# Kernel tuning notes

Measured on AMD Instinct MI355X. Metric: run time of the kernel, lower is better.

Reference implementation:

```python
import jax, jax.numpy as jnp
import numpy as np

LATENT, U_DIM, NUM_PROD, NUM_INJ, FEAT_C = 128, 30, 20, 10, 128
WELL_IN = LATENT + U_DIM + FEAT_C  # 286
HID = 64
B = 16384


def setup_inputs() -> dict:
    key = jax.random.key(0)
    ks = jax.random.split(key, 12)
    s = lambda fan_in: 1.0 / np.sqrt(fan_in)
    return {
        "zt": jax.random.normal(ks[0], (B, LATENT), jnp.float32),
        "dt": 1,
        "ut": jax.random.normal(ks[1], (B, U_DIM), jnp.float32),
        "well_features": jax.random.normal(ks[2], (B, NUM_PROD, FEAT_C), jnp.float32),
        # StructuredODEFunc params: dz/dt = -(L L^T) z + Bm u
        "L": jax.random.normal(ks[3], (LATENT, LATENT), jnp.float32) * s(LATENT),
        "Bm": jax.random.normal(ks[4], (LATENT, U_DIM), jnp.float32) * s(U_DIM),
        # per-well MLP heads, stacked: [P, in, out]
        "W1": jax.random.uniform(ks[5], (NUM_PROD, WELL_IN, HID), jnp.float32, -s(WELL_IN), s(WELL_IN)),
        "b1": jax.random.uniform(ks[6], (NUM_PROD, HID), jnp.float32, -s(WELL_IN), s(WELL_IN)),
        "W2": jax.random.uniform(ks[7], (NUM_PROD, HID, 2), jnp.float32, -s(HID), s(HID)),
        "b2": jax.random.uniform(ks[8], (NUM_PROD, 2), jnp.float32, -s(HID), s(HID)),
        # injector head: Linear(latent+u_dim, num_inj)
        "Wi": jax.random.uniform(ks[9], (LATENT + U_DIM, NUM_INJ), jnp.float32, -s(LATENT + U_DIM), s(LATENT + U_DIM)),
        "bi": jax.random.uniform(ks[10], (NUM_INJ,), jnp.float32, -s(LATENT + U_DIM), s(LATENT + U_DIM)),
    }


def reference(zt, dt, ut, well_features, L, Bm, W1, b1, W2, b2, Wi, bi):
    # ODE step: A = -L L^T, f(z) = A z + Bm u; euler over t_span [0,1] -> one step h=1
    A = -(L @ L.T)                                  # [D, D]
    zt1 = zt + zt @ A.T + ut @ Bm.T                 # [B, D]
    zu = jnp.concatenate([zt1, ut], axis=-1)        # [B, D+U]
    # per-well heads, fused as batched gather-MLP
    zu_b = jnp.broadcast_to(zu[:, None, :], (zu.shape[0], NUM_PROD, zu.shape[1]))
    head_in = jnp.concatenate([zu_b, well_features], axis=-1)        # [B, P, WELL_IN]
    h = jax.nn.relu(jnp.einsum('bpi,pih->bph', head_in, W1) + b1)    # [B, P, 64]
    well_out = jnp.einsum('bph,pho->bpo', h, W2) + b2                # [B, P, 2]
    well_out = well_out.reshape(well_out.shape[0], NUM_PROD * 2)     # concat order matches loop
    inj_out = zu @ Wi + bi                                           # [B, num_inj]
    yt1 = jnp.concatenate([well_out, inj_out], axis=-1)              # [B, 2P+I]
    return zt1, yt1
```

## Files before the change

kernel.cpp:

```cpp
#include <hip/hip_runtime.h>

#define BATCH   16384
#define LATENT  128
#define U_DIM   30
#define NUM_PROD 20
#define NUM_INJ 10
#define FEAT_C  128
#define WELL_IN 286
#define HID     64
#define ZT1_N   (BATCH*LATENT)
#define OUT_ROW (NUM_PROD*2+NUM_INJ)

typedef unsigned short u16;
typedef __attribute__((ext_vector_type(8))) short  short8;
typedef __attribute__((ext_vector_type(4))) float  floatx4;

__device__ __forceinline__ u16 f2bf(float f){
    unsigned x = __builtin_bit_cast(unsigned, f);
    x += 0x7fffu + ((x >> 16) & 1u);
    return (u16)(x >> 16);
}
__device__ __forceinline__ short8 cvt8(floatx4 a, floatx4 b){
    short8 s;
    s[0]=(short)f2bf(a[0]); s[1]=(short)f2bf(a[1]);
    s[2]=(short)f2bf(a[2]); s[3]=(short)f2bf(a[3]);
    s[4]=(short)f2bf(b[0]); s[5]=(short)f2bf(b[1]);
    s[6]=(short)f2bf(b[2]); s[7]=(short)f2bf(b[3]);
    return s;
}

#define NW1  368640
#define NGS  20480
#define NWIS 2560
#define NW2S 20480
__device__ u16 g_w1s[NW1];
__device__ u16 g_gs [NGS];
__device__ u16 g_wis[NWIS];
__device__ u16 g_w2s[NW2S];

__global__ __launch_bounds__(256) void prep_kernel(
    const float* __restrict__ L, const float* __restrict__ Bm,
    const float* __restrict__ W1, const float* __restrict__ Wi,
    const float* __restrict__ W2)
{
    const int bx = blockIdx.x, t = threadIdx.x;
    if (bx < 180) {
        int s = bx*256 + t;
        int lane = s & 63;
        int rest = s >> 6;
        int kk = rest % 9, pn = rest / 9;
        int n0 = pn & 3, p = pn >> 2;
        int kbase = kk*32 + ((lane>>4)*8);
        int n = n0*16 + (lane & 15);
        short8 v;
#pragma unroll
        for (int j = 0; j < 8; j++) {
            int k = kbase + j;
            u16 b = 0;
            if (k < 158)        b = f2bf(W1[(p*WELL_IN + k)*HID + n]);
            else if (k >= 160)  b = f2bf(W1[(p*WELL_IN + (k-2))*HID + n]);
            v[j] = (short)b;
        }
        *(short8*)&g_w1s[(size_t)s*8] = v;
        return;
    }
    if (bx < 272) {
        int sid = (bx-180)*256 + t;
        if (sid < NW2S) {
            int j=sid&7, lane=(sid>>3)&63, rest=sid>>9;
            int kk=rest&1, p=rest>>1;
            int k=kk*32+((lane>>4)*8)+j, n=lane&15;
            g_w2s[sid] = (n<2) ? f2bf(W2[(p*HID+k)*2+n]) : (u16)0;
            return;
        }
        sid -= NW2S;
        if (sid < NWIS) {
            int j=sid&7, lane=(sid>>3)&63, kk=sid>>9;
            int k=kk*32+((lane>>4)*8)+j, n=lane&15;
            g_wis[sid] = (k<158 && n<NUM_INJ) ? f2bf(Wi[k*NUM_INJ+n]) : (u16)0;
            return;
        }
        sid -= NWIS;
        if (sid < 512) {
            int lane=sid&63, nt=sid>>6;
            int q=lane>>4, n=nt*16+(lane&15);
#pragma unroll
            for (int j = 0; j < 8; j++) {
                int u = q*8 + j;
                float v = (u < U_DIM) ? Bm[n*U_DIM + u] : 0.f;
                g_gs[((nt*5+4)*64 + lane)*8 + j] = f2bf(v);
            }
        }
        return;
    }
    const int mt = bx - 272;
    const int w = t>>6, lane=t&63, q=lane>>4, m=lane&15;
    floatx4 accG[2];
    accG[0]=(floatx4){0.f,0.f,0.f,0.f}; accG[1]=(floatx4){0.f,0.f,0.f,0.f};
#pragma unroll
    for (int kk = 0; kk < 4; kk++) {
        const float* ap = &L[(mt*16+m)*128 + kk*32 + q*8];
        short8 a = cvt8(*(const floatx4*)ap, *(const floatx4*)(ap+4));
#pragma unroll
        for (int ntl = 0; ntl < 2; ntl++) {
            int nt = w*2 + ntl;
            const float* bp = &L[(nt*16+m)*128 + kk*32 + q*8];
            short8 b = cvt8(*(const floatx4*)bp, *(const floatx4*)(bp+4));
            accG[ntl] = __builtin_amdgcn_mfma_f32_16x16x32_bf16(a, b, accG[ntl], 0, 0, 0);
        }
    }
#pragma unroll
    for (int ntl = 0; ntl < 2; ntl++)
#pragma unroll
        for (int r = 0; r < 4; r++) {
            int kg = mt*16 + q*4 + r;
            int n  = (w*2+ntl)*16 + m;
            float v = ((kg==n) ? 1.f : 0.f) - accG[ntl][r];
            int fi = ((n>>4)*5 + (kg>>5))*512 + (((kg>>3)&3)*16 + (n&15))*8 + (kg&7);
            g_gs[fi] = f2bf(v);
        }
}

__global__ __launch_bounds__(256) void ker_main(
    const float* __restrict__ zt, const float* __restrict__ ut,
    const float* __restrict__ wff, const float* __restrict__ b1,
    const float* __restrict__ b2,  const float* __restrict__ bi,
    float* __restrict__ outf)
{
    __shared__ alignas(16) u16   zus[32][168];
    __shared__ alignas(16) u16   wfb0[4096];
    __shared__ alignas(16) u16   wfb1[4096];
    __shared__ alignas(16) u16   hs[32][72];
    __shared__ alignas(16) float outs[32][50];
    const int t = threadIdx.x;
    const int row0 = blockIdx.x * 32;
    const int w = t >> 6, lane = t & 63, q = lane >> 4, m = lane & 15;

    const int lane_s = t & 63, cs = (t >> 6) & 3;
    const int qs = lane_s >> 4, ms = lane_s & 15;

    floatx4 rA[4], rB[4];
    auto issue = [&](floatx4 (&r)[4], int p){
#pragma unroll
        for (int rt = 0; rt < 2; rt++) {
            const float* pb = &wff[((size_t)(row0 + rt*16 + ms)*NUM_PROD + p)*FEAT_C + cs*32 + qs*8];
            r[rt*2+0] = *(const floatx4*)pb;
            r[rt*2+1] = *(const floatx4*)(pb + 4);
        }
    };
    auto cstore = [&](const floatx4 (&r)[4], u16* __restrict__ wfb){
        *(short8*)&wfb[((size_t)(0*4 + cs)*64 + lane_s)*8] = cvt8(r[0], r[1]);
        *(short8*)&wfb[((size_t)(1*4 + cs)*64 + lane_s)*8] = cvt8(r[2], r[3]);
    };

    issue(rA, 0);
    issue(rB, 1);

    for (int i = t; i < 1024; i += 256) {
        int r = i >> 5, c4 = i & 31;
        floatx4 v = *(const floatx4*)&zt[(size_t)(row0 + r)*128 + c4*4];
        u16* d = &zus[r][c4*4];
        d[0]=f2bf(v[0]); d[1]=f2bf(v[1]); d[2]=f2bf(v[2]); d[3]=f2bf(v[3]);
    }
    for (int i = t; i < 32*U_DIM; i += 256) {
        int r = i / U_DIM, c = i - r*U_DIM;
        zus[r][128 + c] = f2bf(ut[(row0 + r)*U_DIM + c]);
    }
    if (t < 64) {
        zus[t >> 1][158 + (t & 1)] = 0;
    }
    __syncthreads();

    {
        const int mt = w & 1, ng = (w >> 1) * 4;
        floatx4 acc[4];
#pragma unroll
        for (int c = 0; c < 4; c++) acc[c] = (floatx4){0.f,0.f,0.f,0.f};
#pragma unroll
        for (int kk = 0; kk < 5; kk++) {
            short8 a = *(const short8*)&zus[mt*16 + m][kk*32 + q*8];
#pragma unroll
            for (int c = 0; c < 4; c++) {
                short8 b = *(const short8*)&g_gs[(((ng+c)*5 + kk)*64 + lane)*8];
                acc[c] = __builtin_amdgcn_mfma_f32_16x16x32_bf16(a, b, acc[c], 0, 0, 0);
            }
        }
        __syncthreads();
#pragma unroll
        for (int c = 0; c < 4; c++)
#pragma unroll
            for (int r = 0; r < 4; r++) {
                int row = mt*16 + q*4 + r;
                int col = (ng+c)*16 + m;
                float v = acc[c][r];
                outf[(size_t)(row0 + row)*128 + col] = v;
                zus[row][col] = f2bf(v);
            }
    }
    __syncthreads();

    if (w == 3) {
        floatx4 ai[2];
        ai[0]=(floatx4){0.f,0.f,0.f,0.f}; ai[1]=(floatx4){0.f,0.f,0.f,0.f};
#pragma unroll
        for (int kk = 0; kk < 5; kk++) {
            short8 b = *(const short8*)&g_wis[(kk*64 + lane)*8];
#pragma unroll
            for (int rt = 0; rt < 2; rt++) {
                short8 a = *(const short8*)&zus[rt*16 + m][kk*32 + q*8];
                ai[rt] = __builtin_amdgcn_mfma_f32_16x16x32_bf16(a, b, ai[rt], 0, 0, 0);
            }
        }
        if (m < NUM_INJ) {
            float bv = bi[m];
#pragma unroll
            for (int rt = 0; rt < 2; rt++)
#pragma unroll
                for (int r = 0; r < 4; r++)
                    outs[rt*16 + q*4 + r][40 + m] = ai[rt][r] + bv;
        }
    }

    auto do_well = [&](int p, const u16* __restrict__ wfb){
        const u16* w1p = g_w1s + (size_t)p * 4 * 9 * 64 * 8;
        short8 bfr[9];
#pragma unroll
        for (int kk = 0; kk < 9; kk++)
            bfr[kk] = *(const short8*)&w1p[((size_t)(w*9 + kk)*64 + lane)*8];
        floatx4 acc0 = (floatx4){0.f,0.f,0.f,0.f};
        floatx4 acc1 = (floatx4){0.f,0.f,0.f,0.f};
#pragma unroll
        for (int kk = 0; kk < 9; kk++) {
            short8 a0, a1;
            if (kk < 5) {
                a0 = *(const short8*)&zus[m][kk*32 + q*8];
                a1 = *(const short8*)&zus[16 + m][kk*32 + q*8];
            } else {
                a0 = *(const short8*)&wfb[((size_t)(0*4 + kk-5)*64 + lane)*8];
                a1 = *(const short8*)&wfb[((size_t)(1*4 + kk-5)*64 + lane)*8];
            }
            acc0 = __builtin_amdgcn_mfma_f32_16x16x32_bf16(a0, bfr[kk], acc0, 0, 0, 0);
            acc1 = __builtin_amdgcn_mfma_f32_16x16x32_bf16(a1, bfr[kk], acc1, 0, 0, 0);
        }
        {
            int col = w*16 + m;
            float bb = b1[p*HID + col];
#pragma unroll
            for (int rt = 0; rt < 2; rt++) {
                floatx4 a = rt ? acc1 : acc0;
#pragma unroll
                for (int r = 0; r < 4; r++) {
                    float v = a[r] + bb;
                    v = v > 0.f ? v : 0.f;
                    hs[rt*16 + q*4 + r][col] = f2bf(v);
                }
            }
        }
        __syncthreads();
        if (w < 2) {
            floatx4 a2 = (floatx4){0.f,0.f,0.f,0.f};
#pragma unroll
            for (int kk2 = 0; kk2 < 2; kk2++) {
                short8 a = *(const short8*)&hs[16*w + m][kk2*32 + q*8];
                short8 b = *(const short8*)&g_w2s[((size_t)(p*2 + kk2)*64 + lane)*8];
                a2 = __builtin_amdgcn_mfma_f32_16x16x32_bf16(a, b, a2, 0, 0, 0);
            }
            if (m < 2) {
                float bb = b2[p*2 + m];
#pragma unroll
                for (int r = 0; r < 4; r++)
                    outs[16*w + q*4 + r][p*2 + m] = a2[r] + bb;
            }
        }
    };

    for (int tb = 0; tb < 20; tb += 2) {
        cstore(rA, wfb0);
        __syncthreads();
        if (tb + 2 < 20) issue(rA, tb + 2);
        do_well(tb, wfb0);
        cstore(rB, wfb1);
        __syncthreads();
        if (tb + 3 < 20) issue(rB, tb + 3);
        do_well(tb + 1, wfb1);
    }
    __syncthreads();

    {
        const float* of = &outs[0][0];
        float* dst = outf + (size_t)ZT1_N + (size_t)row0 * OUT_ROW;
        for (int i = t; i < 400; i += 256)
            *(floatx4*)&dst[i*4] = *(const floatx4*)&of[i*4];
    }
}

extern "C" void kernel_launch(void* const* d_in, const int* in_sizes, int n_in,
                              void* d_out, int out_size, void* d_ws, size_t ws_size,
                              hipStream_t stream)
{
    const float* zt = (const float*)d_in[0];
    const float* ut = (const float*)d_in[2];
    const float* wf = (const float*)d_in[3];
    const float* L  = (const float*)d_in[4];
    const float* Bm = (const float*)d_in[5];
    const float* W1 = (const float*)d_in[6];
    const float* b1 = (const float*)d_in[7];
    const float* W2 = (const float*)d_in[8];
    const float* b2 = (const float*)d_in[9];
    const float* Wi = (const float*)d_in[10];
    const float* bi = (const float*)d_in[11];
    float* outf = (float*)d_out;

    prep_kernel<<<280, 256, 0, stream>>>(L, Bm, W1, Wi, W2);
    ker_main<<<512, 256, 0, stream>>>(zt, ut, wf, b1, b2, bi, outf);
}
```

Measured before the change: 303.1 us.

## Double block size, compute second well layer via shuffles and prefetch W1 fragments

Doubles the threads per block to 512 so each wave handles one 16-row tile of a 16-column slice of the hidden layer. The second MLP layer is computed in fp32 via lane shuffle reductions and LDS atomics, replacing the hs staging buffer, its extra barrier per well and the MFMA pass. W1 B-fragments for the next well are prefetched into registers, and W2, b1 and b2 are staged in LDS up front. This raises register pressure from the double-buffered fragments, adds atomic contention on LDS, and with only 512 blocks occupancy depends on the larger blocks fitting.

New measurement: 322.4 us. 1.06x slower.

```diff
diff --git a/kernel.cpp b/kernel.cpp
--- a/kernel.cpp
+++ b/kernel.cpp
@@ -121,73 +121,76 @@
         }
 }
 
-__global__ __launch_bounds__(256) void ker_main(
+__global__ __launch_bounds__(512) void ker_main(
     const float* __restrict__ zt, const float* __restrict__ ut,
     const float* __restrict__ wff, const float* __restrict__ b1,
     const float* __restrict__ b2,  const float* __restrict__ bi,
+    const float* __restrict__ W2g,
     float* __restrict__ outf)
 {
     __shared__ alignas(16) u16   zus[32][168];
     __shared__ alignas(16) u16   wfb0[4096];
     __shared__ alignas(16) u16   wfb1[4096];
-    __shared__ alignas(16) u16   hs[32][72];
     __shared__ alignas(16) float outs[32][50];
+    __shared__ alignas(16) float w2l[2560];
+    __shared__ alignas(16) float b1l[1280];
     const int t = threadIdx.x;
     const int row0 = blockIdx.x * 32;
     const int w = t >> 6, lane = t & 63, q = lane >> 4, m = lane & 15;
-
-    const int lane_s = t & 63, cs = (t >> 6) & 3;
+    const int n0 = w & 3, rt = w >> 2;
+
+    const int lane_s = t & 63, cs = (t >> 6) & 3, rts = t >> 8;
     const int qs = lane_s >> 4, ms = lane_s & 15;
 
-    floatx4 rA[4], rB[4];
-    auto issue = [&](floatx4 (&r)[4], int p){
-#pragma unroll
-        for (int rt = 0; rt < 2; rt++) {
-            const float* pb = &wff[((size_t)(row0 + rt*16 + ms)*NUM_PROD + p)*FEAT_C + cs*32 + qs*8];
-            r[rt*2+0] = *(const floatx4*)pb;
-            r[rt*2+1] = *(const floatx4*)(pb + 4);
-        }
+    floatx4 rA[2], rB[2];
+    auto issue = [&](floatx4 (&r)[2], int p){
+        const float* pb = &wff[((size_t)(row0 + rts*16 + ms)*NUM_PROD + p)*FEAT_C + cs*32 + qs*8];
+        r[0] = *(const floatx4*)pb;
+        r[1] = *(const floatx4*)(pb + 4);
     };
-    auto cstore = [&](const floatx4 (&r)[4], u16* __restrict__ wfb){
-        *(short8*)&wfb[((size_t)(0*4 + cs)*64 + lane_s)*8] = cvt8(r[0], r[1]);
-        *(short8*)&wfb[((size_t)(1*4 + cs)*64 + lane_s)*8] = cvt8(r[2], r[3]);
+    auto cstore = [&](const floatx4 (&r)[2], u16* __restrict__ wfb){
+        *(short8*)&wfb[((rts*4 + cs)*64 + lane_s)*8] = cvt8(r[0], r[1]);
     };
 
     issue(rA, 0);
     issue(rB, 1);
 
-    for (int i = t; i < 1024; i += 256) {
+    for (int i = t; i < 1024; i += 512) {
         int r = i >> 5, c4 = i & 31;
         floatx4 v = *(const floatx4*)&zt[(size_t)(row0 + r)*128 + c4*4];
         u16* d = &zus[r][c4*4];
         d[0]=f2bf(v[0]); d[1]=f2bf(v[1]); d[2]=f2bf(v[2]); d[3]=f2bf(v[3]);
     }
-    for (int i = t; i < 32*U_DIM; i += 256) {
+    for (int i = t; i < 32*U_DIM; i += 512) {
         int r = i / U_DIM, c = i - r*U_DIM;
         zus[r][128 + c] = f2bf(ut[(row0 + r)*U_DIM + c]);
     }
-    if (t < 64) {
-        zus[t >> 1][158 + (t & 1)] = 0;
+    if (t < 64) zus[t >> 1][158 + (t & 1)] = 0;
+    for (int i = t; i < 2560; i += 512) w2l[i] = W2g[i];
+    for (int i = t; i < 1280; i += 512) b1l[i] = b1[i];
+    for (int i = t; i < 1600; i += 512) {
+        int col = i % 50;
+        (&outs[0][0])[i] = (col < 40) ? b2[col] : 0.f;
     }
     __syncthreads();
 
     {
-        const int mt = w & 1, ng = (w >> 1) * 4;
-        floatx4 acc[4];
-#pragma unroll
-        for (int c = 0; c < 4; c++) acc[c] = (floatx4){0.f,0.f,0.f,0.f};
+        const int mt = w & 1, ng = (w >> 1) * 2;
+        floatx4 acc[2];
+        acc[0] = (floatx4){0.f,0.f,0.f,0.f};
+        acc[1] = (floatx4){0.f,0.f,0.f,0.f};
 #pragma unroll
         for (int kk = 0; kk < 5; kk++) {
             short8 a = *(const short8*)&zus[mt*16 + m][kk*32 + q*8];
 #pragma unroll
-            for (int c = 0; c < 4; c++) {
+            for (int c = 0; c < 2; c++) {
                 short8 b = *(const short8*)&g_gs[(((ng+c)*5 + kk)*64 + lane)*8];
                 acc[c] = __builtin_amdgcn_mfma_f32_16x16x32_bf16(a, b, acc[c], 0, 0, 0);
             }
         }
         __syncthreads();
 #pragma unroll
-        for (int c = 0; c < 4; c++)
+        for (int c = 0; c < 2; c++)
 #pragma unroll
             for (int r = 0; r < 4; r++) {
                 int row = mt*16 + q*4 + r;
@@ -199,97 +202,83 @@
     }
     __syncthreads();
 
-    if (w == 3) {
-        floatx4 ai[2];
-        ai[0]=(floatx4){0.f,0.f,0.f,0.f}; ai[1]=(floatx4){0.f,0.f,0.f,0.f};
+    short8 za[5];
+#pragma unroll
+    for (int kk = 0; kk < 5; kk++)
+        za[kk] = *(const short8*)&zus[rt*16 + m][kk*32 + q*8];
+
+    if (n0 == 3) {
+        floatx4 ai = (floatx4){0.f,0.f,0.f,0.f};
 #pragma unroll
         for (int kk = 0; kk < 5; kk++) {
             short8 b = *(const short8*)&g_wis[(kk*64 + lane)*8];
-#pragma unroll
-            for (int rt = 0; rt < 2; rt++) {
-                short8 a = *(const short8*)&zus[rt*16 + m][kk*32 + q*8];
-                ai[rt] = __builtin_amdgcn_mfma_f32_16x16x32_bf16(a, b, ai[rt], 0, 0, 0);
-            }
+            ai = __builtin_amdgcn_mfma_f32_16x16x32_bf16(za[kk], b, ai, 0, 0, 0);
         }
         if (m < NUM_INJ) {
             float bv = bi[m];
 #pragma unroll
-            for (int rt = 0; rt < 2; rt++)
-#pragma unroll
-                for (int r = 0; r < 4; r++)
-                    outs[rt*16 + q*4 + r][40 + m] = ai[rt][r] + bv;
-        }
-    }
-
-    auto do_well = [&](int p, const u16* __restrict__ wfb){
-        const u16* w1p = g_w1s + (size_t)p * 4 * 9 * 64 * 8;
-        short8 bfr[9];
+            for (int r = 0; r < 4; r++)
+                outs[rt*16 + q*4 + r][40 + m] = ai[r] + bv;
+        }
+    }
+
+    short8 bfrA[9], bfrB[9];
+    auto loadB = [&](short8 (&bfr)[9], int p){
 #pragma unroll
         for (int kk = 0; kk < 9; kk++)
-            bfr[kk] = *(const short8*)&w1p[((size_t)(w*9 + kk)*64 + lane)*8];
-        floatx4 acc0 = (floatx4){0.f,0.f,0.f,0.f};
-        floatx4 acc1 = (floatx4){0.f,0.f,0.f,0.f};
+            bfr[kk] = *(const short8*)&g_w1s[(((size_t)p*36 + n0*9 + kk)*64 + lane)*8];
+    };
+    loadB(bfrA, 0);
+
+    auto do_well = [&](int p, const u16* __restrict__ wfb,
+                       const short8 (&bfrC)[9], short8 (&bfrN)[9]){
+        if (p < 19) loadB(bfrN, p + 1);
+        floatx4 acc = (floatx4){0.f,0.f,0.f,0.f};
 #pragma unroll
         for (int kk = 0; kk < 9; kk++) {
-            short8 a0, a1;
-            if (kk < 5) {
-                a0 = *(const short8*)&zus[m][kk*32 + q*8];
-                a1 = *(const short8*)&zus[16 + m][kk*32 + q*8];
-            } else {
-                a0 = *(const short8*)&wfb[((size_t)(0*4 + kk-5)*64 + lane)*8];
-                a1 = *(const short8*)&wfb[((size_t)(1*4 + kk-5)*64 + lane)*8];
-            }
-            acc0 = __builtin_amdgcn_mfma_f32_16x16x32_bf16(a0, bfr[kk], acc0, 0, 0, 0);
-            acc1 = __builtin_amdgcn_mfma_f32_16x16x32_bf16(a1, bfr[kk], acc1, 0, 0, 0);
-        }
-        {
-            int col = w*16 + m;
-            float bb = b1[p*HID + col];
-#pragma unroll
-            for (int rt = 0; rt < 2; rt++) {
-                floatx4 a = rt ? acc1 : acc0;
-#pragma unroll
-                for (int r = 0; r < 4; r++) {
-                    float v = a[r] + bb;
-                    v = v > 0.f ? v : 0.f;
-                    hs[rt*16 + q*4 + r][col] = f2bf(v);
-                }
-            }
-        }
-        __syncthreads();
-        if (w < 2) {
-            floatx4 a2 = (floatx4){0.f,0.f,0.f,0.f};
-#pragma unroll
-            for (int kk2 = 0; kk2 < 2; kk2++) {
-                short8 a = *(const short8*)&hs[16*w + m][kk2*32 + q*8];
-                short8 b = *(const short8*)&g_w2s[((size_t)(p*2 + kk2)*64 + lane)*8];
-                a2 = __builtin_amdgcn_mfma_f32_16x16x32_bf16(a, b, a2, 0, 0, 0);
-            }
-            if (m < 2) {
-                float bb = b2[p*2 + m];
-#pragma unroll
-                for (int r = 0; r < 4; r++)
-                    outs[16*w + q*4 + r][p*2 + m] = a2[r] + bb;
-            }
-        }
+            short8 a = (kk < 5) ? za[kk]
+                     : *(const short8*)&wfb[((rt*4 + kk-5)*64 + lane)*8];
+            acc = __builtin_amdgcn_mfma_f32_16x16x32_bf16(a, bfrC[kk], acc, 0, 0, 0);
+        }
+        const int col = n0*16 + m;
+        const float bb = b1l[p*64 + col];
+        const float w2x = w2l[(p*64 + col)*2 + 0];
+        const float w2y = w2l[(p*64 + col)*2 + 1];
+        float s[8];
+#pragma unroll
+        for (int r = 0; r < 4; r++) {
+            float h = acc[r] + bb;
+            h = h > 0.f ? h : 0.f;
+            s[r*2+0] = h * w2x;
+            s[r*2+1] = h * w2y;
+        }
+#pragma unroll
+        for (int mask = 1; mask < 16; mask <<= 1)
+#pragma unroll
+            for (int i = 0; i < 8; i++)
+                s[i] += __shfl_xor(s[i], mask);
+        float val = (m==0)?s[0]:(m==1)?s[1]:(m==2)?s[2]:(m==3)?s[3]
+                   :(m==4)?s[4]:(m==5)?s[5]:(m==6)?s[6]:s[7];
+        if (m < 8)
+            atomicAdd(&outs[rt*16 + q*4 + (m>>1)][p*2 + (m&1)], val);
     };
 
     for (int tb = 0; tb < 20; tb += 2) {
         cstore(rA, wfb0);
         __syncthreads();
         if (tb + 2 < 20) issue(rA, tb + 2);
-        do_well(tb, wfb0);
+        do_well(tb, wfb0, bfrA, bfrB);
         cstore(rB, wfb1);
         __syncthreads();
         if (tb + 3 < 20) issue(rB, tb + 3);
-        do_well(tb + 1, wfb1);
+        do_well(tb + 1, wfb1, bfrB, bfrA);
     }
     __syncthreads();
 
     {
         const float* of = &outs[0][0];
         float* dst = outf + (size_t)ZT1_N + (size_t)row0 * OUT_ROW;
-        for (int i = t; i < 400; i += 256)
+        for (int i = t; i < 400; i += 512)
             *(floatx4*)&dst[i*4] = *(const floatx4*)&of[i*4];
     }
 }
@@ -312,5 +301,5 @@
     float* outf = (float*)d_out;
 
     prep_kernel<<<280, 256, 0, stream>>>(L, Bm, W1, Wi, W2);
-    ker_main<<<512, 256, 0, stream>>>(zt, ut, wf, b1, b2, bi, outf);
-}
+    ker_main<<<512, 512, 0, stream>>>(zt, ut, wf, b1, b2, bi, W2, outf);
+}
```
